# Kernel optimization log

Hardware: AMD Instinct MI355X
Metric: run time of the kernel (lower is better)

## Reference

```python
import jax, jax.numpy as jnp
import numpy as np

B, D, C = 2048, 1024, 8192


def setup_inputs() -> dict:
    key = jax.random.key(0)
    k1, k2, k3 = jax.random.split(key, 3)
    x = jax.random.normal(k1, (B, D), dtype=jnp.float32)
    y = jax.random.randint(k2, (B,), 0, C)
    centroids = jax.random.normal(k3, (C, D), dtype=jnp.float32)
    return {"x": x, "y": y, "centroids": centroids}


def reference(x, y, centroids):
    x2 = jnp.sum(x * x, axis=-1, keepdims=True)          # (B, 1)
    c2 = jnp.sum(centroids * centroids, axis=-1)          # (C,)
    logits = -(x2 + c2[None, :] - 2.0 * (x @ centroids.T))  # (B, C)
    decisions = jnp.argmax(logits, axis=1)                # nearest centroid
    score = jnp.mean((decisions == y).astype(jnp.float32))
    # CrossEntropyLoss(distances, y)
    logp = jax.nn.log_softmax(logits, axis=-1)
    loss = -jnp.mean(jnp.take_along_axis(logp, y[:, None], axis=1))
    return loss, score
```

## Files before the change

### kernel.cpp

```cpp
#include <hip/hip_runtime.h>
#include <cstdint>

#define MDIM 2048
#define KDIM 1024
#define CDIM 8192
#define BM 256
#define BN 256
#define BK 32
#define NT (KDIM / BK)
#define NCHUNK (CDIM / 64)
#define CVT_BLOCKS 1280

typedef __attribute__((ext_vector_type(8))) __bf16 bf16x8;
typedef __attribute__((ext_vector_type(4))) float f32x4;

__device__ __forceinline__ unsigned short f2bf(float f) {
  unsigned u = __float_as_uint(f);
  u += 0x7fffu + ((u >> 16) & 1u);
  return (unsigned short)(u >> 16);
}

__device__ __forceinline__ void async_ld16(const void* g, void* l) {
  __builtin_amdgcn_global_load_lds(
      (__attribute__((address_space(1))) void*)(g),
      (__attribute__((address_space(3))) void*)(l),
      16, 0, 0);
}

__global__ __launch_bounds__(256) void convert_all(const float* __restrict__ x,
                                                   const float* __restrict__ cent,
                                                   unsigned short* __restrict__ xb,
                                                   unsigned short* __restrict__ cb,
                                                   float* __restrict__ c2) {
  const int t = threadIdx.x;
  __shared__ float red[4];
  for (int b = blockIdx.x; b < MDIM + CDIM; b += CVT_BLOCKS) {
    if (b < MDIM) {
      const float4 v = ((const float4*)(x + (size_t)b * KDIM))[t];
      ushort4 o;
      o.x = f2bf(v.x); o.y = f2bf(v.y); o.z = f2bf(v.z); o.w = f2bf(v.w);
      ((ushort4*)(xb + (size_t)b * KDIM))[t] = o;
    } else {
      const int row = b - MDIM;
      const float4 v = ((const float4*)(cent + (size_t)row * KDIM))[t];
      ushort4 o;
      o.x = f2bf(v.x); o.y = f2bf(v.y); o.z = f2bf(v.z); o.w = f2bf(v.w);
      ((ushort4*)(cb + (size_t)row * KDIM))[t] = o;
      float p = v.x * v.x + v.y * v.y + v.z * v.z + v.w * v.w;
      for (int d = 32; d; d >>= 1) p += __shfl_down(p, d, 64);
      if ((t & 63) == 0) red[t >> 6] = p;
      __syncthreads();
      if (t == 0) c2[row] = red[0] + red[1] + red[2] + red[3];
      __syncthreads();
    }
  }
}

__global__ __launch_bounds__(512, 2) void gemm_reduce(
    const unsigned short* __restrict__ Ab, const unsigned short* __restrict__ Bb,
    const float* __restrict__ c2,
    float* __restrict__ pm, float* __restrict__ pl, int* __restrict__ pidx) {
  __shared__ __align__(16) char lds[4 * 32768];

  const int tid = threadIdx.x;
  const int wave = tid >> 6, lane = tid & 63;
  const int wm = wave >> 2, wn = wave & 3;
  const int quad = lane >> 4, c16 = lane & 15;

  const int id = blockIdx.y * gridDim.x + blockIdx.x;
  const int lid = (id & 7) * 32 + (id >> 3);
  const int bm = lid >> 5, bn = lid & 31;
  const int bmBase = bm * BM, bnBase = bn * BN;

  const int r1 = tid >> 2, c1 = (tid & 3) ^ ((r1 >> 1) & 3);
  const int r2 = (tid + 512) >> 2, c2s = (tid & 3) ^ ((r2 >> 1) & 3);
  const char* Ag1 = (const char*)(Ab + (size_t)(bmBase + r1) * KDIM + c1 * 8);
  const char* Ag2 = (const char*)(Ab + (size_t)(bmBase + r2) * KDIM + c2s * 8);
  const char* Bg1 = (const char*)(Bb + (size_t)(bnBase + r1) * KDIM + c1 * 8);
  const char* Bg2 = (const char*)(Bb + (size_t)(bnBase + r2) * KDIM + c2s * 8);
  const int wbyte = wave * 1024;

  int aoff[8], boff[4];
#pragma unroll
  for (int mt = 0; mt < 8; ++mt) {
    const int row = wm * 128 + mt * 16 + c16;
    aoff[mt] = row * 64 + ((quad ^ ((row >> 1) & 3)) * 16);
  }
#pragma unroll
  for (int nt = 0; nt < 4; ++nt) {
    const int col = wn * 64 + nt * 16 + c16;
    boff[nt] = col * 64 + ((quad ^ ((col >> 1) & 3)) * 16);
  }

  f32x4 acc[8][4] = {};

#define STAGE(T)                                          \
  {                                                       \
    const int _ko = (T) * (BK * 2);                       \
    char* _sb = &lds[((T) & 3) * 32768];                  \
    async_ld16(Ag1 + _ko, _sb + wbyte);                   \
    async_ld16(Ag2 + _ko, _sb + 8192 + wbyte);            \
    async_ld16(Bg1 + _ko, _sb + 16384 + wbyte);           \
    async_ld16(Bg2 + _ko, _sb + 24576 + wbyte);           \
  }

  STAGE(0); STAGE(1); STAGE(2);

#pragma unroll 1
  for (int t = 0; t < NT; ++t) {
    if (t < NT - 2)       asm volatile("s_waitcnt vmcnt(8)" ::: "memory");
    else if (t == NT - 2) asm volatile("s_waitcnt vmcnt(4)" ::: "memory");
    else                  asm volatile("s_waitcnt vmcnt(0)" ::: "memory");
    __builtin_amdgcn_s_barrier();
    __builtin_amdgcn_sched_barrier(0);

    const char* sb = &lds[(t & 3) * 32768];
    bf16x8 a[8], b[4];
#pragma unroll
    for (int mt = 0; mt < 8; ++mt) a[mt] = *(const bf16x8*)(sb + aoff[mt]);
#pragma unroll
    for (int nt = 0; nt < 4; ++nt) b[nt] = *(const bf16x8*)(sb + 16384 + boff[nt]);

    if (t < NT - 3) STAGE(t + 3);

    asm volatile("s_waitcnt lgkmcnt(0)" ::: "memory");
    __builtin_amdgcn_sched_barrier(0);
    __builtin_amdgcn_s_setprio(1);
#pragma unroll
    for (int mt = 0; mt < 8; ++mt)
#pragma unroll
      for (int nt = 0; nt < 4; ++nt)
        acc[mt][nt] = __builtin_amdgcn_mfma_f32_16x16x32_bf16(a[mt], b[nt], acc[mt][nt], 0, 0, 0);
    __builtin_amdgcn_s_setprio(0);
  }
#undef STAGE

  const int colbase = bnBase + wn * 64;
  float c2v[4];
#pragma unroll
  for (int nt = 0; nt < 4; ++nt) c2v[nt] = c2[colbase + nt * 16 + c16];

  const int chunk = bn * 4 + wn;
#pragma unroll
  for (int mt = 0; mt < 8; ++mt) {
#pragma unroll
    for (int r = 0; r < 4; ++r) {
      float sv[4];
#pragma unroll
      for (int nt = 0; nt < 4; ++nt) sv[nt] = 2.0f * acc[mt][nt][r] - c2v[nt];
      float m = sv[0];
      int idx = colbase + c16;
#pragma unroll
      for (int nt = 1; nt < 4; ++nt) {
        if (sv[nt] > m) { m = sv[nt]; idx = colbase + nt * 16 + c16; }
      }
      float l = 0.f;
#pragma unroll
      for (int nt = 0; nt < 4; ++nt) l += __expf(sv[nt] - m);
      for (int d = 1; d < 16; d <<= 1) {
        float om = __shfl_xor(m, d, 64);
        float ol = __shfl_xor(l, d, 64);
        int oi = __shfl_xor(idx, d, 64);
        float M = fmaxf(m, om);
        l = l * __expf(m - M) + ol * __expf(om - M);
        idx = (om > m || (om == m && oi < idx)) ? oi : idx;
        m = M;
      }
      if (c16 == 0) {
        const int row = bmBase + wm * 128 + mt * 16 + quad * 4 + r;
        pm[(size_t)row * NCHUNK + chunk] = m;
        pl[(size_t)row * NCHUNK + chunk] = l;
        pidx[(size_t)row * NCHUNK + chunk] = idx;
      }
    }
  }
}

__global__ __launch_bounds__(128) void combine_kernel(
    const float* __restrict__ pm, const float* __restrict__ pl,
    const int* __restrict__ pidx, const float* __restrict__ x,
    const float* __restrict__ cent, const float* __restrict__ c2,
    const int* __restrict__ y,
    float* __restrict__ loss_part, float* __restrict__ corr_part) {
  const int row = blockIdx.x, t = threadIdx.x;
  const int yc = y[row];

  float m = pm[(size_t)row * NCHUNK + t];
  float l = pl[(size_t)row * NCHUNK + t];
  int idx = pidx[(size_t)row * NCHUNK + t];

  const float4* xa = (const float4*)(x + (size_t)row * KDIM) + t * 2;
  const float4* ca = (const float4*)(cent + (size_t)yc * KDIM) + t * 2;
  const float4 a0 = xa[0], a1 = xa[1], b0 = ca[0], b1 = ca[1];
  float dot = a0.x * b0.x + a0.y * b0.y + a0.z * b0.z + a0.w * b0.w
            + a1.x * b1.x + a1.y * b1.y + a1.z * b1.z + a1.w * b1.w;

  for (int d = 1; d < 64; d <<= 1) {
    const float om = __shfl_xor(m, d, 64);
    const float ol = __shfl_xor(l, d, 64);
    const int oi = __shfl_xor(idx, d, 64);
    const float od = __shfl_xor(dot, d, 64);
    const float M = fmaxf(m, om);
    l = l * __expf(m - M) + ol * __expf(om - M);
    idx = (om > m || (om == m && oi < idx)) ? oi : idx;
    m = M;
    dot += od;
  }
  __shared__ float sm[2], sl[2], sd[2];
  __shared__ int si[2];
  if ((t & 63) == 0) { sm[t >> 6] = m; sl[t >> 6] = l; si[t >> 6] = idx; sd[t >> 6] = dot; }
  __syncthreads();
  if (t == 0) {
    const float m0 = sm[0], m1 = sm[1];
    const float M = fmaxf(m0, m1);
    const float L = sl[0] * __expf(m0 - M) + sl[1] * __expf(m1 - M);
    int g;
    if (m1 > m0 || (m1 == m0 && si[1] < si[0])) g = si[1]; else g = si[0];
    const float sy = 2.0f * (sd[0] + sd[1]) - c2[yc];
    loss_part[row] = __logf(L) + M - sy;
    corr_part[row] = (g == yc) ? 1.f : 0.f;
  }
}

__global__ __launch_bounds__(256) void finalize(const float* __restrict__ loss_part,
                                                const float* __restrict__ corr_part,
                                                float* __restrict__ out) {
  const int t = threadIdx.x;
  float s0 = 0.f, s1 = 0.f;
  for (int i = t; i < MDIM; i += 256) { s0 += loss_part[i]; s1 += corr_part[i]; }
  for (int d = 32; d; d >>= 1) {
    s0 += __shfl_down(s0, d, 64);
    s1 += __shfl_down(s1, d, 64);
  }
  __shared__ float r0[4], r1[4];
  if ((t & 63) == 0) { r0[t >> 6] = s0; r1[t >> 6] = s1; }
  __syncthreads();
  if (t == 0) {
    out[0] = (r0[0] + r0[1] + r0[2] + r0[3]) * (1.0f / MDIM);
    out[1] = (r1[0] + r1[1] + r1[2] + r1[3]) * (1.0f / MDIM);
  }
}

extern "C" void kernel_launch(void* const* d_in, const int* in_sizes, int n_in,
                              void* d_out, int out_size, void* d_ws, size_t ws_size,
                              hipStream_t stream) {
  const float* x = (const float*)d_in[0];
  const int* y = (const int*)d_in[1];
  const float* cent = (const float*)d_in[2];
  float* out = (float*)d_out;

  char* ws = (char*)d_ws;
  const size_t OFF_XB = 0;
  const size_t OFF_CB = OFF_XB + (size_t)MDIM * KDIM * 2;
  const size_t OFF_C2 = OFF_CB + (size_t)CDIM * KDIM * 2;
  const size_t OFF_PM = OFF_C2 + (size_t)CDIM * 4;
  const size_t OFF_PL = OFF_PM + (size_t)NCHUNK * MDIM * 4;
  const size_t OFF_PI = OFF_PL + (size_t)NCHUNK * MDIM * 4;
  const size_t OFF_LP = OFF_PI + (size_t)NCHUNK * MDIM * 4;
  const size_t OFF_CP = OFF_LP + (size_t)MDIM * 4;
  const size_t NEED = OFF_CP + (size_t)MDIM * 4;
  if (ws_size < NEED) return;

  unsigned short* xb = (unsigned short*)(ws + OFF_XB);
  unsigned short* cb = (unsigned short*)(ws + OFF_CB);
  float* c2 = (float*)(ws + OFF_C2);
  float* pm = (float*)(ws + OFF_PM);
  float* pl = (float*)(ws + OFF_PL);
  int* pidx = (int*)(ws + OFF_PI);
  float* loss_part = (float*)(ws + OFF_LP);
  float* corr_part = (float*)(ws + OFF_CP);

  convert_all<<<CVT_BLOCKS, 256, 0, stream>>>(x, cent, xb, cb, c2);
  gemm_reduce<<<dim3(CDIM / BN, MDIM / BM), 512, 0, stream>>>(xb, cb, c2, pm, pl, pidx);
  combine_kernel<<<MDIM, 128, 0, stream>>>(pm, pl, pidx, x, cent, c2, y, loss_part, corr_part);
  finalize<<<1, 256, 0, stream>>>(loss_part, corr_part, out);
}
```

Before: 137.8 us.

## Fuse convert, GEMM, combine and finalize into one cooperative persistent kernel

Merges the four separate launches into a single cooperative kernel of 256 blocks, with grid-wide syncs between the bf16 conversion, GEMM-with-row-reduction, per-row combine, and final mean phases. This removes three kernel launch gaps and their tail effects. In exchange, each phase now runs at a fixed 256-block geometry, which is less parallel for the conversion and combine phases, and the grid syncs add their own cost. Co-residency of all 256 blocks relies on two blocks per CU, matching the launch bounds.

```diff
diff --git a/kernel.cpp b/kernel.cpp
--- a/kernel.cpp
+++ b/kernel.cpp
@@ -1,4 +1,5 @@
 #include <hip/hip_runtime.h>
+#include <hip/hip_cooperative_groups.h>
 #include <cstdint>
 
 #define MDIM 2048
@@ -9,7 +10,6 @@
 #define BK 32
 #define NT (KDIM / BK)
 #define NCHUNK (CDIM / 64)
-#define CVT_BLOCKS 1280
 
 typedef __attribute__((ext_vector_type(8))) __bf16 bf16x8;
 typedef __attribute__((ext_vector_type(4))) float f32x4;
@@ -27,217 +27,244 @@
       16, 0, 0);
 }
 
-__global__ __launch_bounds__(256) void convert_all(const float* __restrict__ x,
-                                                   const float* __restrict__ cent,
-                                                   unsigned short* __restrict__ xb,
-                                                   unsigned short* __restrict__ cb,
-                                                   float* __restrict__ c2) {
-  const int t = threadIdx.x;
-  __shared__ float red[4];
-  for (int b = blockIdx.x; b < MDIM + CDIM; b += CVT_BLOCKS) {
-    if (b < MDIM) {
-      const float4 v = ((const float4*)(x + (size_t)b * KDIM))[t];
-      ushort4 o;
-      o.x = f2bf(v.x); o.y = f2bf(v.y); o.z = f2bf(v.z); o.w = f2bf(v.w);
-      ((ushort4*)(xb + (size_t)b * KDIM))[t] = o;
-    } else {
-      const int row = b - MDIM;
-      const float4 v = ((const float4*)(cent + (size_t)row * KDIM))[t];
-      ushort4 o;
-      o.x = f2bf(v.x); o.y = f2bf(v.y); o.z = f2bf(v.z); o.w = f2bf(v.w);
-      ((ushort4*)(cb + (size_t)row * KDIM))[t] = o;
-      float p = v.x * v.x + v.y * v.y + v.z * v.z + v.w * v.w;
-      for (int d = 32; d; d >>= 1) p += __shfl_down(p, d, 64);
-      if ((t & 63) == 0) red[t >> 6] = p;
+__global__ __launch_bounds__(512, 2) void fused_all(
+    const float* __restrict__ x, const int* __restrict__ y,
+    const float* __restrict__ cent,
+    unsigned short* __restrict__ xb, unsigned short* __restrict__ cb,
+    float* __restrict__ c2,
+    float* __restrict__ pm, float* __restrict__ pl, int* __restrict__ pidx,
+    float* __restrict__ loss_part, float* __restrict__ corr_part,
+    float* __restrict__ out) {
+  __shared__ __align__(16) char lds[4 * 32768];
+  cooperative_groups::grid_group grid = cooperative_groups::this_grid();
+  const int tid = threadIdx.x;
+  const int bid = blockIdx.x;
+
+  {
+    const int rt = tid & 255;
+    const int half = tid >> 8;
+    float* red = (float*)lds;
+    for (int s = 0; s < 20; ++s) {
+      const int row = bid * 40 + s * 2 + half;
+      const bool isc = row >= MDIM;
+      if (!isc) {
+        const float4 v = ((const float4*)(x + (size_t)row * KDIM))[rt];
+        ushort4 o;
+        o.x = f2bf(v.x); o.y = f2bf(v.y); o.z = f2bf(v.z); o.w = f2bf(v.w);
+        ((ushort4*)(xb + (size_t)row * KDIM))[rt] = o;
+      } else {
+        const int r = row - MDIM;
+        const float4 v = ((const float4*)(cent + (size_t)r * KDIM))[rt];
+        ushort4 o;
+        o.x = f2bf(v.x); o.y = f2bf(v.y); o.z = f2bf(v.z); o.w = f2bf(v.w);
+        ((ushort4*)(cb + (size_t)r * KDIM))[rt] = o;
+        float p = v.x * v.x + v.y * v.y + v.z * v.z + v.w * v.w;
+        for (int d = 32; d; d >>= 1) p += __shfl_down(p, d, 64);
+        if ((rt & 63) == 0) red[half * 4 + (rt >> 6)] = p;
+      }
       __syncthreads();
-      if (t == 0) c2[row] = red[0] + red[1] + red[2] + red[3];
+      if (isc && rt == 0) {
+        const int r = row - MDIM;
+        c2[r] = red[half * 4 + 0] + red[half * 4 + 1] + red[half * 4 + 2] + red[half * 4 + 3];
+      }
       __syncthreads();
     }
   }
-}
-
-__global__ __launch_bounds__(512, 2) void gemm_reduce(
-    const unsigned short* __restrict__ Ab, const unsigned short* __restrict__ Bb,
-    const float* __restrict__ c2,
-    float* __restrict__ pm, float* __restrict__ pl, int* __restrict__ pidx) {
-  __shared__ __align__(16) char lds[4 * 32768];
-
-  const int tid = threadIdx.x;
-  const int wave = tid >> 6, lane = tid & 63;
-  const int wm = wave >> 2, wn = wave & 3;
-  const int quad = lane >> 4, c16 = lane & 15;
-
-  const int id = blockIdx.y * gridDim.x + blockIdx.x;
-  const int lid = (id & 7) * 32 + (id >> 3);
-  const int bm = lid >> 5, bn = lid & 31;
-  const int bmBase = bm * BM, bnBase = bn * BN;
-
-  const int r1 = tid >> 2, c1 = (tid & 3) ^ ((r1 >> 1) & 3);
-  const int r2 = (tid + 512) >> 2, c2s = (tid & 3) ^ ((r2 >> 1) & 3);
-  const char* Ag1 = (const char*)(Ab + (size_t)(bmBase + r1) * KDIM + c1 * 8);
-  const char* Ag2 = (const char*)(Ab + (size_t)(bmBase + r2) * KDIM + c2s * 8);
-  const char* Bg1 = (const char*)(Bb + (size_t)(bnBase + r1) * KDIM + c1 * 8);
-  const char* Bg2 = (const char*)(Bb + (size_t)(bnBase + r2) * KDIM + c2s * 8);
-  const int wbyte = wave * 1024;
-
-  int aoff[8], boff[4];
-#pragma unroll
-  for (int mt = 0; mt < 8; ++mt) {
-    const int row = wm * 128 + mt * 16 + c16;
-    aoff[mt] = row * 64 + ((quad ^ ((row >> 1) & 3)) * 16);
+  __threadfence();
+  grid.sync();
+  __threadfence();
+
+  {
+    const int wave = tid >> 6, lane = tid & 63;
+    const int wm = wave >> 2, wn = wave & 3;
+    const int quad = lane >> 4, c16 = lane & 15;
+
+    const int id = bid;
+    const int lid = (id & 7) * 32 + (id >> 3);
+    const int bm = lid >> 5, bn = lid & 31;
+    const int bmBase = bm * BM, bnBase = bn * BN;
+
+    const int r1 = tid >> 2, c1 = (tid & 3) ^ ((r1 >> 1) & 3);
+    const int r2 = (tid + 512) >> 2, c2s = (tid & 3) ^ ((r2 >> 1) & 3);
+    const char* Ag1 = (const char*)(xb + (size_t)(bmBase + r1) * KDIM + c1 * 8);
+    const char* Ag2 = (const char*)(xb + (size_t)(bmBase + r2) * KDIM + c2s * 8);
+    const char* Bg1 = (const char*)(cb + (size_t)(bnBase + r1) * KDIM + c1 * 8);
+    const char* Bg2 = (const char*)(cb + (size_t)(bnBase + r2) * KDIM + c2s * 8);
+    const int wbyte = wave * 1024;
+
+    int aoff[8], boff[4];
+#pragma unroll
+    for (int mt = 0; mt < 8; ++mt) {
+      const int row = wm * 128 + mt * 16 + c16;
+      aoff[mt] = row * 64 + ((quad ^ ((row >> 1) & 3)) * 16);
+    }
+#pragma unroll
+    for (int nt = 0; nt < 4; ++nt) {
+      const int col = wn * 64 + nt * 16 + c16;
+      boff[nt] = col * 64 + ((quad ^ ((col >> 1) & 3)) * 16);
+    }
+
+    f32x4 acc[8][4] = {};
+
+#define STAGE(T)                                          \
+    {                                                     \
+      const int _ko = (T) * (BK * 2);                     \
+      char* _sb = &lds[((T) & 3) * 32768];                \
+      async_ld16(Ag1 + _ko, _sb + wbyte);                 \
+      async_ld16(Ag2 + _ko, _sb + 8192 + wbyte);          \
+      async_ld16(Bg1 + _ko, _sb + 16384 + wbyte);         \
+      async_ld16(Bg2 + _ko, _sb + 24576 + wbyte);         \
+    }
+
+    STAGE(0); STAGE(1); STAGE(2);
+
+#pragma unroll 1
+    for (int t = 0; t < NT; ++t) {
+      if (t < NT - 2)       asm volatile("s_waitcnt vmcnt(8)" ::: "memory");
+      else if (t == NT - 2) asm volatile("s_waitcnt vmcnt(4)" ::: "memory");
+      else                  asm volatile("s_waitcnt vmcnt(0)" ::: "memory");
+      __builtin_amdgcn_s_barrier();
+      __builtin_amdgcn_sched_barrier(0);
+
+      const char* sb = &lds[(t & 3) * 32768];
+      bf16x8 a[8], b[4];
+#pragma unroll
+      for (int mt = 0; mt < 8; ++mt) a[mt] = *(const bf16x8*)(sb + aoff[mt]);
+#pragma unroll
+      for (int nt = 0; nt < 4; ++nt) b[nt] = *(const bf16x8*)(sb + 16384 + boff[nt]);
+
+      if (t < NT - 3) STAGE(t + 3);
+
+      asm volatile("s_waitcnt lgkmcnt(0)" ::: "memory");
+      __builtin_amdgcn_sched_barrier(0);
+      __builtin_amdgcn_s_setprio(1);
+#pragma unroll
+      for (int mt = 0; mt < 8; ++mt)
+#pragma unroll
+        for (int nt = 0; nt < 4; ++nt)
+          acc[mt][nt] = __builtin_amdgcn_mfma_f32_16x16x32_bf16(a[mt], b[nt], acc[mt][nt], 0, 0, 0);
+      __builtin_amdgcn_s_setprio(0);
+    }
+#undef STAGE
+
+    const int colbase = bnBase + wn * 64;
+    float c2v[4];
+#pragma unroll
+    for (int nt = 0; nt < 4; ++nt) c2v[nt] = c2[colbase + nt * 16 + c16];
+
+    const int chunk = bn * 4 + wn;
+#pragma unroll
+    for (int mt = 0; mt < 8; ++mt) {
+#pragma unroll
+      for (int r = 0; r < 4; ++r) {
+        float sv[4];
+#pragma unroll
+        for (int nt = 0; nt < 4; ++nt) sv[nt] = 2.0f * acc[mt][nt][r] - c2v[nt];
+        float m = sv[0];
+        int idx = colbase + c16;
+#pragma unroll
+        for (int nt = 1; nt < 4; ++nt) {
+          if (sv[nt] > m) { m = sv[nt]; idx = colbase + nt * 16 + c16; }
+        }
+        float l = 0.f;
+#pragma unroll
+        for (int nt = 0; nt < 4; ++nt) l += __expf(sv[nt] - m);
+        for (int d = 1; d < 16; d <<= 1) {
+          float om = __shfl_xor(m, d, 64);
+          float ol = __shfl_xor(l, d, 64);
+          int oi = __shfl_xor(idx, d, 64);
+          float M = fmaxf(m, om);
+          l = l * __expf(m - M) + ol * __expf(om - M);
+          idx = (om > m || (om == m && oi < idx)) ? oi : idx;
+          m = M;
+        }
+        if (c16 == 0) {
+          const int row = bmBase + wm * 128 + mt * 16 + quad * 4 + r;
+          pm[(size_t)row * NCHUNK + chunk] = m;
+          pl[(size_t)row * NCHUNK + chunk] = l;
+          pidx[(size_t)row * NCHUNK + chunk] = idx;
+        }
+      }
+    }
   }
-#pragma unroll
-  for (int nt = 0; nt < 4; ++nt) {
-    const int col = wn * 64 + nt * 16 + c16;
-    boff[nt] = col * 64 + ((quad ^ ((col >> 1) & 3)) * 16);
-  }
-
-  f32x4 acc[8][4] = {};
-
-#define STAGE(T)                                          \
-  {                                                       \
-    const int _ko = (T) * (BK * 2);                       \
-    char* _sb = &lds[((T) & 3) * 32768];                  \
-    async_ld16(Ag1 + _ko, _sb + wbyte);                   \
-    async_ld16(Ag2 + _ko, _sb + 8192 + wbyte);            \
-    async_ld16(Bg1 + _ko, _sb + 16384 + wbyte);           \
-    async_ld16(Bg2 + _ko, _sb + 24576 + wbyte);           \
-  }
-
-  STAGE(0); STAGE(1); STAGE(2);
-
-#pragma unroll 1
-  for (int t = 0; t < NT; ++t) {
-    if (t < NT - 2)       asm volatile("s_waitcnt vmcnt(8)" ::: "memory");
-    else if (t == NT - 2) asm volatile("s_waitcnt vmcnt(4)" ::: "memory");
-    else                  asm volatile("s_waitcnt vmcnt(0)" ::: "memory");
-    __builtin_amdgcn_s_barrier();
-    __builtin_amdgcn_sched_barrier(0);
-
-    const char* sb = &lds[(t & 3) * 32768];
-    bf16x8 a[8], b[4];
-#pragma unroll
-    for (int mt = 0; mt < 8; ++mt) a[mt] = *(const bf16x8*)(sb + aoff[mt]);
-#pragma unroll
-    for (int nt = 0; nt < 4; ++nt) b[nt] = *(const bf16x8*)(sb + 16384 + boff[nt]);
-
-    if (t < NT - 3) STAGE(t + 3);
-
-    asm volatile("s_waitcnt lgkmcnt(0)" ::: "memory");
-    __builtin_amdgcn_sched_barrier(0);
-    __builtin_amdgcn_s_setprio(1);
-#pragma unroll
-    for (int mt = 0; mt < 8; ++mt)
-#pragma unroll
-      for (int nt = 0; nt < 4; ++nt)
-        acc[mt][nt] = __builtin_amdgcn_mfma_f32_16x16x32_bf16(a[mt], b[nt], acc[mt][nt], 0, 0, 0);
-    __builtin_amdgcn_s_setprio(0);
-  }
-#undef STAGE
-
-  const int colbase = bnBase + wn * 64;
-  float c2v[4];
-#pragma unroll
-  for (int nt = 0; nt < 4; ++nt) c2v[nt] = c2[colbase + nt * 16 + c16];
-
-  const int chunk = bn * 4 + wn;
-#pragma unroll
-  for (int mt = 0; mt < 8; ++mt) {
-#pragma unroll
-    for (int r = 0; r < 4; ++r) {
-      float sv[4];
-#pragma unroll
-      for (int nt = 0; nt < 4; ++nt) sv[nt] = 2.0f * acc[mt][nt][r] - c2v[nt];
-      float m = sv[0];
-      int idx = colbase + c16;
-#pragma unroll
-      for (int nt = 1; nt < 4; ++nt) {
-        if (sv[nt] > m) { m = sv[nt]; idx = colbase + nt * 16 + c16; }
-      }
-      float l = 0.f;
-#pragma unroll
-      for (int nt = 0; nt < 4; ++nt) l += __expf(sv[nt] - m);
-      for (int d = 1; d < 16; d <<= 1) {
-        float om = __shfl_xor(m, d, 64);
-        float ol = __shfl_xor(l, d, 64);
-        int oi = __shfl_xor(idx, d, 64);
-        float M = fmaxf(m, om);
+  __threadfence();
+  grid.sync();
+  __threadfence();
+
+  {
+    const int grp = tid >> 7;
+    const int t = tid & 127;
+    float* smA = (float*)lds;
+    float* slA = smA + 8;
+    float* sdA = slA + 8;
+    int*   siA = (int*)(sdA + 8);
+    for (int it = 0; it < 2; ++it) {
+      const int row = bid * 8 + it * 4 + grp;
+      const int yc = y[row];
+
+      float m = pm[(size_t)row * NCHUNK + t];
+      float l = pl[(size_t)row * NCHUNK + t];
+      int idx = pidx[(size_t)row * NCHUNK + t];
+
+      const float4* xa = (const float4*)(x + (size_t)row * KDIM) + t * 2;
+      const float4* ca = (const float4*)(cent + (size_t)yc * KDIM) + t * 2;
+      const float4 a0 = xa[0], a1 = xa[1], b0 = ca[0], b1 = ca[1];
+      float dot = a0.x * b0.x + a0.y * b0.y + a0.z * b0.z + a0.w * b0.w
+                + a1.x * b1.x + a1.y * b1.y + a1.z * b1.z + a1.w * b1.w;
+
+      for (int d = 1; d < 64; d <<= 1) {
+        const float om = __shfl_xor(m, d, 64);
+        const float ol = __shfl_xor(l, d, 64);
+        const int oi = __shfl_xor(idx, d, 64);
+        const float od = __shfl_xor(dot, d, 64);
+        const float M = fmaxf(m, om);
         l = l * __expf(m - M) + ol * __expf(om - M);
         idx = (om > m || (om == m && oi < idx)) ? oi : idx;
         m = M;
-      }
-      if (c16 == 0) {
-        const int row = bmBase + wm * 128 + mt * 16 + quad * 4 + r;
-        pm[(size_t)row * NCHUNK + chunk] = m;
-        pl[(size_t)row * NCHUNK + chunk] = l;
-        pidx[(size_t)row * NCHUNK + chunk] = idx;
-      }
+        dot += od;
+      }
+      const int wv = t >> 6;
+      if ((t & 63) == 0) {
+        smA[grp * 2 + wv] = m; slA[grp * 2 + wv] = l;
+        siA[grp * 2 + wv] = idx; sdA[grp * 2 + wv] = dot;
+      }
+      __syncthreads();
+      if (t == 0) {
+        const float m0 = smA[grp * 2], m1 = smA[grp * 2 + 1];
+        const float M = fmaxf(m0, m1);
+        const float L = slA[grp * 2] * __expf(m0 - M) + slA[grp * 2 + 1] * __expf(m1 - M);
+        int g;
+        if (m1 > m0 || (m1 == m0 && siA[grp * 2 + 1] < siA[grp * 2])) g = siA[grp * 2 + 1];
+        else g = siA[grp * 2];
+        const float sy = 2.0f * (sdA[grp * 2] + sdA[grp * 2 + 1]) - c2[yc];
+        loss_part[row] = __logf(L) + M - sy;
+        corr_part[row] = (g == yc) ? 1.f : 0.f;
+      }
+      __syncthreads();
     }
   }
-}
-
-__global__ __launch_bounds__(128) void combine_kernel(
-    const float* __restrict__ pm, const float* __restrict__ pl,
-    const int* __restrict__ pidx, const float* __restrict__ x,
-    const float* __restrict__ cent, const float* __restrict__ c2,
-    const int* __restrict__ y,
-    float* __restrict__ loss_part, float* __restrict__ corr_part) {
-  const int row = blockIdx.x, t = threadIdx.x;
-  const int yc = y[row];
-
-  float m = pm[(size_t)row * NCHUNK + t];
-  float l = pl[(size_t)row * NCHUNK + t];
-  int idx = pidx[(size_t)row * NCHUNK + t];
-
-  const float4* xa = (const float4*)(x + (size_t)row * KDIM) + t * 2;
-  const float4* ca = (const float4*)(cent + (size_t)yc * KDIM) + t * 2;
-  const float4 a0 = xa[0], a1 = xa[1], b0 = ca[0], b1 = ca[1];
-  float dot = a0.x * b0.x + a0.y * b0.y + a0.z * b0.z + a0.w * b0.w
-            + a1.x * b1.x + a1.y * b1.y + a1.z * b1.z + a1.w * b1.w;
-
-  for (int d = 1; d < 64; d <<= 1) {
-    const float om = __shfl_xor(m, d, 64);
-    const float ol = __shfl_xor(l, d, 64);
-    const int oi = __shfl_xor(idx, d, 64);
-    const float od = __shfl_xor(dot, d, 64);
-    const float M = fmaxf(m, om);
-    l = l * __expf(m - M) + ol * __expf(om - M);
-    idx = (om > m || (om == m && oi < idx)) ? oi : idx;
-    m = M;
-    dot += od;
-  }
-  __shared__ float sm[2], sl[2], sd[2];
-  __shared__ int si[2];
-  if ((t & 63) == 0) { sm[t >> 6] = m; sl[t >> 6] = l; si[t >> 6] = idx; sd[t >> 6] = dot; }
-  __syncthreads();
-  if (t == 0) {
-    const float m0 = sm[0], m1 = sm[1];
-    const float M = fmaxf(m0, m1);
-    const float L = sl[0] * __expf(m0 - M) + sl[1] * __expf(m1 - M);
-    int g;
-    if (m1 > m0 || (m1 == m0 && si[1] < si[0])) g = si[1]; else g = si[0];
-    const float sy = 2.0f * (sd[0] + sd[1]) - c2[yc];
-    loss_part[row] = __logf(L) + M - sy;
-    corr_part[row] = (g == yc) ? 1.f : 0.f;
-  }
-}
-
-__global__ __launch_bounds__(256) void finalize(const float* __restrict__ loss_part,
-                                                const float* __restrict__ corr_part,
-                                                float* __restrict__ out) {
-  const int t = threadIdx.x;
-  float s0 = 0.f, s1 = 0.f;
-  for (int i = t; i < MDIM; i += 256) { s0 += loss_part[i]; s1 += corr_part[i]; }
-  for (int d = 32; d; d >>= 1) {
-    s0 += __shfl_down(s0, d, 64);
-    s1 += __shfl_down(s1, d, 64);
-  }
-  __shared__ float r0[4], r1[4];
-  if ((t & 63) == 0) { r0[t >> 6] = s0; r1[t >> 6] = s1; }
-  __syncthreads();
-  if (t == 0) {
-    out[0] = (r0[0] + r0[1] + r0[2] + r0[3]) * (1.0f / MDIM);
-    out[1] = (r1[0] + r1[1] + r1[2] + r1[3]) * (1.0f / MDIM);
+  __threadfence();
+  grid.sync();
+  __threadfence();
+
+  if (bid == 0) {
+    float s0 = 0.f, s1 = 0.f;
+    for (int i = tid; i < MDIM; i += 512) { s0 += loss_part[i]; s1 += corr_part[i]; }
+    for (int d = 32; d; d >>= 1) {
+      s0 += __shfl_down(s0, d, 64);
+      s1 += __shfl_down(s1, d, 64);
+    }
+    float* r0 = (float*)lds;
+    float* r1 = r0 + 8;
+    if ((tid & 63) == 0) { r0[tid >> 6] = s0; r1[tid >> 6] = s1; }
+    __syncthreads();
+    if (tid == 0) {
+      float a = 0.f, b = 0.f;
+#pragma unroll
+      for (int w = 0; w < 8; ++w) { a += r0[w]; b += r1[w]; }
+      out[0] = a * (1.0f / MDIM);
+      out[1] = b * (1.0f / MDIM);
+    }
   }
 }
 
@@ -270,8 +297,19 @@
   float* loss_part = (float*)(ws + OFF_LP);
   float* corr_part = (float*)(ws + OFF_CP);
 
-  convert_all<<<CVT_BLOCKS, 256, 0, stream>>>(x, cent, xb, cb, c2);
-  gemm_reduce<<<dim3(CDIM / BN, MDIM / BM), 512, 0, stream>>>(xb, cb, c2, pm, pl, pidx);
-  combine_kernel<<<MDIM, 128, 0, stream>>>(pm, pl, pidx, x, cent, c2, y, loss_part, corr_part);
-  finalize<<<1, 256, 0, stream>>>(loss_part, corr_part, out);
+  void* args[12];
+  args[0] = (void*)&x;
+  args[1] = (void*)&y;
+  args[2] = (void*)&cent;
+  args[3] = (void*)&xb;
+  args[4] = (void*)&cb;
+  args[5] = (void*)&c2;
+  args[6] = (void*)&pm;
+  args[7] = (void*)&pl;
+  args[8] = (void*)&pidx;
+  args[9] = (void*)&loss_part;
+  args[10] = (void*)&corr_part;
+  args[11] = (void*)&out;
+
+  hipLaunchCooperativeKernel(fused_all, dim3(256), dim3(512), args, 0, stream);
 }
```

New measurement: 451.0 us. 227% more time.
